# Kernel optimization log

Hardware: AMD Instinct MI355X
Metric: run time of the kernel (lower is better)

Reference implementation:

```python
import jax, jax.numpy as jnp
import numpy as np

DIM = 1280
HEADS = 16
HEAD_DIM = DIM // HEADS  # 80
SEQ = 2048


def setup_inputs() -> dict:
    key = jax.random.key(0)
    ks = jax.random.split(key, 6)
    hidden_states = jax.random.normal(ks[0], (SEQ, DIM), jnp.float32)
    rotary_pos_emb = jax.random.normal(ks[1], (SEQ, HEAD_DIM // 2), jnp.float32)
    # 4 variable-length windows packed into one flat sequence
    cu_seqlens = jnp.array([0, 512, 1024, 1536, 2048], jnp.int32)
    w_scale = DIM ** -0.5
    qkv_w = jax.random.normal(ks[2], (3 * DIM, DIM), jnp.float32) * w_scale
    qkv_b = jax.random.normal(ks[3], (3 * DIM,), jnp.float32) * 0.01
    proj_w = jax.random.normal(ks[4], (DIM, DIM), jnp.float32) * w_scale
    proj_b = jax.random.normal(ks[5], (DIM,), jnp.float32) * 0.01
    return {
        "hidden_states": hidden_states,
        "rotary_pos_emb": rotary_pos_emb,
        "cu_seqlens": cu_seqlens,
        "qkv_w": qkv_w,
        "qkv_b": qkv_b,
        "proj_w": proj_w,
        "proj_b": proj_b,
    }


def _apply_rope_vision(x, freqs):
    # x: [S, H, D], freqs: [S, D//2]; matches Qwen2-VL apply_rotary_pos_emb_vision
    cos = jnp.concatenate([jnp.cos(freqs), jnp.cos(freqs)], axis=-1)[:, None, :]  # [S,1,D]
    sin = jnp.concatenate([jnp.sin(freqs), jnp.sin(freqs)], axis=-1)[:, None, :]
    x1, x2 = jnp.split(x, 2, axis=-1)
    rot = jnp.concatenate([-x2, x1], axis=-1)  # rotate_half
    return x * cos + rot * sin


def reference(hidden_states, rotary_pos_emb, cu_seqlens, qkv_w, qkv_b, proj_w, proj_b):
    S = hidden_states.shape[0]
    qkv = (hidden_states @ qkv_w.T + qkv_b).reshape(S, 3, HEADS, HEAD_DIM)
    q, k, v = qkv[:, 0], qkv[:, 1], qkv[:, 2]  # each [S, H, D]
    q = _apply_rope_vision(q, rotary_pos_emb)
    k = _apply_rope_vision(k, rotary_pos_emb)
    # varlen attention: tokens attend only within their cu_seqlens window
    seg = jnp.searchsorted(cu_seqlens[1:], jnp.arange(S), side="right")
    mask = seg[:, None] == seg[None, :]  # [S, S]
    scale = HEAD_DIM ** -0.5
    scores = jnp.einsum("shd,thd->hst", q, k) * scale  # [H, S, S]
    scores = jnp.where(mask[None, :, :], scores, jnp.finfo(scores.dtype).min)
    probs = jax.nn.softmax(scores, axis=-1)
    attn = jnp.einsum("hst,thd->shd", probs, v).reshape(S, DIM)
    return attn @ proj_w.T + proj_b
```

## Files before the change

kernel.cpp:

```cpp
#include <hip/hip_runtime.h>


typedef __attribute__((ext_vector_type(8))) short bf16x8;
typedef __attribute__((ext_vector_type(4))) float floatx4;
typedef __attribute__((ext_vector_type(4))) short short4v;
typedef __attribute__((ext_vector_type(8))) short short8v;

static __device__ __forceinline__ short f2bf(float f) {
  union { float f; unsigned u; } v; v.f = f;
  unsigned r = v.u + 0x7FFFu + ((v.u >> 16) & 1u);
  return (short)(r >> 16);
}
static __device__ __forceinline__ float bf2f(short h) {
  union { unsigned u; float f; } v;
  v.u = ((unsigned)(unsigned short)h) << 16;
  return v.f;
}

static __device__ __forceinline__ void gload16(const short* g, short* l) {
  __builtin_amdgcn_global_load_lds(
      (const __attribute__((address_space(1))) unsigned*)g,
      (__attribute__((address_space(3))) unsigned*)l, 16, 0, 0);
}

#define CVT_N1 327680
#define CVT_N2 614400
#define CVT_N3 204800
__global__ __launch_bounds__(256) void cvt3_kernel(const float* __restrict__ s1, short* __restrict__ d1,
                                                   const float* __restrict__ s2, short* __restrict__ d2,
                                                   const float* __restrict__ s3, short* __restrict__ d3) {
  int i = blockIdx.x * 256 + threadIdx.x;
  const float* s; short* d; int j;
  if (i < CVT_N1)                { s = s1; d = d1; j = i; }
  else if (i < CVT_N1 + CVT_N2)  { s = s2; d = d2; j = i - CVT_N1; }
  else                           { s = s3; d = d3; j = i - CVT_N1 - CVT_N2; }
  float4 x = ((const float4*)s)[2 * j];
  float4 y = ((const float4*)s)[2 * j + 1];
  short8v o;
  o[0] = f2bf(x.x); o[1] = f2bf(x.y); o[2] = f2bf(x.z); o[3] = f2bf(x.w);
  o[4] = f2bf(y.x); o[5] = f2bf(y.y); o[6] = f2bf(y.z); o[7] = f2bf(y.w);
  ((short8v*)d)[j] = o;
}

template <int MODE, int BM, int BN>
__global__ __launch_bounds__(256) void gemm_lds(const short* __restrict__ A,
                                                const short* __restrict__ B,
                                                const float* __restrict__ bias,
                                                void* __restrict__ Cout,
                                                short* __restrict__ vt,
                                                int M, int N, int K) {
  constexpr int AR = BM / 64;
  constexpr int BR = BN / 64;
  constexpr int MI = BM / 32;
  constexpr int NJ = BN / 32;
  __shared__ short As[BM * 32];
  __shared__ short Bs[BN * 32];

  const int tid = threadIdx.x;
  const int lane = tid & 63;
  const int wave = tid >> 6;
  const int l15 = lane & 15, quad = lane >> 4;

  const short* gA[AR]; short* lA[AR];
#pragma unroll
  for (int r = 0; r < AR; ++r) {
    int ch = r * 256 + tid;
    gA[r] = A + (size_t)(blockIdx.y * BM + (ch >> 2)) * K + (ch & 3) * 8;
    lA[r] = As + ch * 8;
  }
  const short* gB[BR]; short* lB[BR];
#pragma unroll
  for (int r = 0; r < BR; ++r) {
    int ch = r * 256 + tid;
    gB[r] = B + (size_t)(blockIdx.x * BN + (ch >> 2)) * K + (ch & 3) * 8;
    lB[r] = Bs + ch * 8;
  }

  const int wm = (wave >> 1) * (BM / 2);
  const int wn = (wave & 1) * (BN / 2);

  floatx4 acc[MI][NJ];
#pragma unroll
  for (int i = 0; i < MI; ++i)
#pragma unroll
    for (int j = 0; j < NJ; ++j) acc[i][j] = (floatx4){0.f, 0.f, 0.f, 0.f};

  for (int k0 = 0; k0 < K; k0 += 32) {
#pragma unroll
    for (int r = 0; r < AR; ++r) { gload16(gA[r], lA[r]); gA[r] += 32; }
#pragma unroll
    for (int r = 0; r < BR; ++r) { gload16(gB[r], lB[r]); gB[r] += 32; }
    __syncthreads();

    bf16x8 af[MI], bfr[NJ];
#pragma unroll
    for (int i = 0; i < MI; ++i)
      af[i] = *(const bf16x8*)(As + (wm + i * 16 + l15) * 32 + quad * 8);
#pragma unroll
    for (int j = 0; j < NJ; ++j)
      bfr[j] = *(const bf16x8*)(Bs + (wn + j * 16 + l15) * 32 + quad * 8);
#pragma unroll
    for (int i = 0; i < MI; ++i)
#pragma unroll
      for (int j = 0; j < NJ; ++j)
        acc[i][j] = __builtin_amdgcn_mfma_f32_16x16x32_bf16(af[i], bfr[j], acc[i][j], 0, 0, 0);
    __syncthreads();
  }

  const int bm = blockIdx.y * BM + wm;
  const int bn = blockIdx.x * BN + wn;
#pragma unroll
  for (int j = 0; j < NJ; ++j) {
    const int col = bn + j * 16 + l15;
    const float bs = bias[col];
    if (MODE == 1) {
      float* C = (float*)Cout;
#pragma unroll
      for (int i = 0; i < MI; ++i) {
        const int row0 = bm + i * 16 + quad * 4;
#pragma unroll
        for (int e = 0; e < 4; ++e)
          C[(size_t)(row0 + e) * N + col] = acc[i][j][e] + bs;
      }
    } else {
      if (bn + j * 16 < 2560) {
        short* C = (short*)Cout;
#pragma unroll
        for (int i = 0; i < MI; ++i) {
          const int row0 = bm + i * 16 + quad * 4;
#pragma unroll
          for (int e = 0; e < 4; ++e)
            C[(size_t)(row0 + e) * 2560 + col] = f2bf(acc[i][j][e] + bs);
        }
      } else {
#pragma unroll
        for (int i = 0; i < MI; ++i) {
          const int row0 = bm + i * 16 + quad * 4;
          short4v v;
#pragma unroll
          for (int e = 0; e < 4; ++e) v[e] = f2bf(acc[i][j][e] + bs);
          *(short4v*)(vt + (size_t)(col - 2560) * 2048 + row0) = v;
        }
      }
    }
  }
}

__global__ __launch_bounds__(256) void rope_repack(const short* __restrict__ qkv,
                                                   const float* __restrict__ rot,
                                                   short* __restrict__ qp,
                                                   short* __restrict__ kp) {
  int idx = blockIdx.x * 256 + threadIdx.x;
  int d = idx % 96;
  int t = idx / 96;
  int s = t & 2047;
  int h = t >> 11;
  size_t dst = ((size_t)h * 2048 + s) * 96 + d;
  if (d < 80) {
    int base = s * 2560 + h * 80;
    int df = (d < 40) ? d : d - 40;
    int dp = (d < 40) ? d + 40 : d - 40;
    float fr = rot[s * 40 + df];
    float c = __cosf(fr), sn = __sinf(fr);
    float sgn = (d < 40) ? -1.f : 1.f;
    float xq = bf2f(qkv[base + d]);
    float pq = bf2f(qkv[base + dp]);
    float xk = bf2f(qkv[base + 1280 + d]);
    float pk = bf2f(qkv[base + 1280 + dp]);
    qp[dst] = f2bf((xq * c + sgn * pq * sn) * 0.11180339887498949f);
    kp[dst] = f2bf(xk * c + sgn * pk * sn);
  } else {
    qp[dst] = 0;
    kp[dst] = 0;
  }
}

__global__ __launch_bounds__(256) void attn_kernel(const short* __restrict__ qp,
                                                   const short* __restrict__ kp,
                                                   const short* __restrict__ vt,
                                                   short* __restrict__ attnout) {
  __shared__ short smem[29184];
  short* const Ks[2] = {smem, smem + 12288};
  short* const Vs[2] = {smem, smem + 10240};

  const int tid = threadIdx.x;
  const int lane = tid & 63;
  const int wave = tid >> 6;
  const int l15 = lane & 15, quad = lane >> 4;
  short* const Pw = smem + 20480 + wave * (16 * 136);

  const int g = blockIdx.x;
  const int hs = g & 63;
  const int grp = g >> 6;
  const int head = hs >> 2;
  const int seg = hs & 3;
  const int q0 = seg * 512 + (grp * 4 + wave) * 16;

  const short* qb = qp + ((size_t)head * 2048 + q0 + l15) * 96 + quad * 8;
  bf16x8 aq0 = *(const bf16x8*)qb;
  bf16x8 aq1 = *(const bf16x8*)(qb + 32);
  bf16x8 aq2 = *(const bf16x8*)(qb + 64);

  const short* kbase = kp + ((size_t)head * 2048 + seg * 512) * 96;
  const short* vbase = vt + (size_t)head * 80 * 2048 + seg * 512;

  floatx4 s[32];
  {
#pragma unroll
    for (int r = 0; r < 6; ++r) {
      int idx = r * 256 + tid;
      gload16(kbase + idx * 8, Ks[0] + idx * 8);
    }
#pragma unroll
    for (int c = 0; c < 4; ++c) {
      __syncthreads();
      if (c < 3) {
        const short* src = kbase + (size_t)(c + 1) * 128 * 96;
#pragma unroll
        for (int r = 0; r < 6; ++r) {
          int idx = r * 256 + tid;
          gload16(src + idx * 8, Ks[(c + 1) & 1] + idx * 8);
        }
      }
      const short* kl = Ks[c & 1];
#pragma unroll
      for (int j = 0; j < 8; ++j) {
        const short* kb = kl + (j * 16 + l15) * 96 + quad * 8;
        floatx4 acc = (floatx4){0.f, 0.f, 0.f, 0.f};
        acc = __builtin_amdgcn_mfma_f32_16x16x32_bf16(aq0, *(const bf16x8*)kb, acc, 0, 0, 0);
        acc = __builtin_amdgcn_mfma_f32_16x16x32_bf16(aq1, *(const bf16x8*)(kb + 32), acc, 0, 0, 0);
        acc = __builtin_amdgcn_mfma_f32_16x16x32_bf16(aq2, *(const bf16x8*)(kb + 64), acc, 0, 0, 0);
        s[c * 8 + j] = acc;
      }
    }
  }

  float m[4] = {-1e30f, -1e30f, -1e30f, -1e30f};
#pragma unroll
  for (int j = 0; j < 32; ++j)
#pragma unroll
    for (int e = 0; e < 4; ++e) m[e] = fmaxf(m[e], s[j][e]);
#pragma unroll
  for (int e = 0; e < 4; ++e)
#pragma unroll
    for (int o = 1; o < 16; o <<= 1) m[e] = fmaxf(m[e], __shfl_xor(m[e], o));
  float l[4] = {0.f, 0.f, 0.f, 0.f};
#pragma unroll
  for (int j = 0; j < 32; ++j)
#pragma unroll
    for (int e = 0; e < 4; ++e) {
      float p = __expf(s[j][e] - m[e]);
      s[j][e] = p;
      l[e] += p;
    }
#pragma unroll
  for (int e = 0; e < 4; ++e)
#pragma unroll
    for (int o = 1; o < 16; o <<= 1) l[e] += __shfl_xor(l[e], o);
  float inv[4];
#pragma unroll
  for (int e = 0; e < 4; ++e) inv[e] = 1.f / l[e];

  floatx4 o5[5];
#pragma unroll
  for (int t = 0; t < 5; ++t) o5[t] = (floatx4){0.f, 0.f, 0.f, 0.f};

  __syncthreads();
#pragma unroll
  for (int r = 0; r < 5; ++r) {
    int idx = r * 256 + tid;
    gload16(vbase + (size_t)(idx >> 4) * 2048 + (idx & 15) * 8, Vs[0] + idx * 8);
  }
#pragma unroll
  for (int c = 0; c < 4; ++c) {
    __syncthreads();
    if (c < 3) {
      const short* src = vbase + (c + 1) * 128;
#pragma unroll
      for (int r = 0; r < 5; ++r) {
        int idx = r * 256 + tid;
        gload16(src + (size_t)(idx >> 4) * 2048 + (idx & 15) * 8, Vs[(c + 1) & 1] + idx * 8);
      }
    }
#pragma unroll
    for (int j = 0; j < 8; ++j)
#pragma unroll
      for (int e = 0; e < 4; ++e)
        Pw[(quad * 4 + e) * 136 + j * 16 + l15] = f2bf(s[c * 8 + j][e]);
    const short* vl = Vs[c & 1];
#pragma unroll
    for (int kk = 0; kk < 4; ++kk) {
      bf16x8 ap = *(const bf16x8*)&Pw[l15 * 136 + kk * 32 + quad * 8];
#pragma unroll
      for (int t = 0; t < 5; ++t) {
        bf16x8 bv = *(const bf16x8*)&vl[(t * 16 + l15) * 128 + kk * 32 + quad * 8];
        o5[t] = __builtin_amdgcn_mfma_f32_16x16x32_bf16(ap, bv, o5[t], 0, 0, 0);
      }
    }
  }

#pragma unroll
  for (int t = 0; t < 5; ++t)
#pragma unroll
    for (int e = 0; e < 4; ++e)
      attnout[(size_t)(q0 + quad * 4 + e) * 1280 + head * 80 + t * 16 + l15] =
          f2bf(o5[t][e] * inv[e]);
}

extern "C" void kernel_launch(void* const* d_in, const int* in_sizes, int n_in,
                              void* d_out, int out_size, void* d_ws, size_t ws_size,
                              hipStream_t stream) {
  const float* hidden = (const float*)d_in[0];
  const float* rotary = (const float*)d_in[1];
  const float* qkv_w = (const float*)d_in[3];
  const float* qkv_b = (const float*)d_in[4];
  const float* proj_w = (const float*)d_in[5];
  const float* proj_b = (const float*)d_in[6];
  float* out = (float*)d_out;

  char* w = (char*)d_ws;
  short* hA   = (short*)(w + 0);
  short* w1   = (short*)(w + 5242880);
  short* w2   = (short*)(w + 15073280);
  short* qkvb = (short*)(w + 18350080);
  short* qp   = (short*)(w + 28835840);
  short* kp   = (short*)(w + 35127296);
  short* vt   = (short*)(w + 41418752);
  short* attn = (short*)(w + 46661632);

  cvt3_kernel<<<4480, 256, 0, stream>>>(hidden, hA, qkv_w, w1, proj_w, w2);

  gemm_lds<2, 128, 128><<<dim3(3840 / 128, 2048 / 128), 256, 0, stream>>>(
      hA, w1, qkv_b, (void*)qkvb, vt, 2048, 3840, 1280);

  rope_repack<<<16 * 2048 * 96 / 256, 256, 0, stream>>>(qkvb, rotary, qp, kp);

  attn_kernel<<<512, 256, 0, stream>>>(qp, kp, vt, attn);

  gemm_lds<1, 128, 64><<<dim3(1280 / 64, 2048 / 128), 256, 0, stream>>>(
      attn, w2, proj_b, (void*)out, nullptr, 2048, 1280, 1280);
}
```

Baseline: 186.8 us.

## Double-buffer GEMM LDS tiles with K=64 steps, XOR swizzle, smaller tiles

Rewrites the bf16 MFMA GEMM to double-buffer its shared-memory tiles, so the next K slice is fetched with global_load_lds while the current one is consumed. Each K step grows from 32 to 64, and the LDS layout uses an XOR swizzle on 16-byte chunks to avoid bank conflicts. Both GEMM launches switch to BM=64 tiles, giving more blocks for occupancy. The cost is twice the LDS per block and only one barrier per iteration, which relies on the loads completing before the next barrier.

Result: faster. 178.9 us (-4.2%).

```diff
diff --git a/kernel.cpp b/kernel.cpp
--- a/kernel.cpp
+++ b/kernel.cpp
@@ -43,37 +43,36 @@
 }
 
 template <int MODE, int BM, int BN>
-__global__ __launch_bounds__(256) void gemm_lds(const short* __restrict__ A,
-                                                const short* __restrict__ B,
-                                                const float* __restrict__ bias,
-                                                void* __restrict__ Cout,
-                                                short* __restrict__ vt,
-                                                int M, int N, int K) {
-  constexpr int AR = BM / 64;
-  constexpr int BR = BN / 64;
+__global__ __launch_bounds__(256) void gemm_db(const short* __restrict__ A,
+                                               const short* __restrict__ B,
+                                               const float* __restrict__ bias,
+                                               void* __restrict__ Cout,
+                                               short* __restrict__ vt,
+                                               int M, int N, int K) {
+  constexpr int AR = BM / 32;
+  constexpr int BR = BN / 32;
   constexpr int MI = BM / 32;
   constexpr int NJ = BN / 32;
-  __shared__ short As[BM * 32];
-  __shared__ short Bs[BN * 32];
+  __shared__ short As[2][BM * 64];
+  __shared__ short Bs[2][BN * 64];
 
   const int tid = threadIdx.x;
   const int lane = tid & 63;
   const int wave = tid >> 6;
   const int l15 = lane & 15, quad = lane >> 4;
-
-  const short* gA[AR]; short* lA[AR];
+  const int x7 = l15 & 7;
+
+  size_t aoff[AR];
 #pragma unroll
   for (int r = 0; r < AR; ++r) {
-    int ch = r * 256 + tid;
-    gA[r] = A + (size_t)(blockIdx.y * BM + (ch >> 2)) * K + (ch & 3) * 8;
-    lA[r] = As + ch * 8;
-  }
-  const short* gB[BR]; short* lB[BR];
+    int s = r * 256 + tid, row = s >> 3, c = (s & 7) ^ (row & 7);
+    aoff[r] = (size_t)(blockIdx.y * BM + row) * K + c * 8;
+  }
+  size_t boff[BR];
 #pragma unroll
   for (int r = 0; r < BR; ++r) {
-    int ch = r * 256 + tid;
-    gB[r] = B + (size_t)(blockIdx.x * BN + (ch >> 2)) * K + (ch & 3) * 8;
-    lB[r] = Bs + ch * 8;
+    int s = r * 256 + tid, row = s >> 3, c = (s & 7) ^ (row & 7);
+    boff[r] = (size_t)(blockIdx.x * BN + row) * K + c * 8;
   }
 
   const int wm = (wave >> 1) * (BM / 2);
@@ -85,26 +84,42 @@
 #pragma unroll
     for (int j = 0; j < NJ; ++j) acc[i][j] = (floatx4){0.f, 0.f, 0.f, 0.f};
 
-  for (int k0 = 0; k0 < K; k0 += 32) {
-#pragma unroll
-    for (int r = 0; r < AR; ++r) { gload16(gA[r], lA[r]); gA[r] += 32; }
-#pragma unroll
-    for (int r = 0; r < BR; ++r) { gload16(gB[r], lB[r]); gB[r] += 32; }
+#pragma unroll
+  for (int r = 0; r < AR; ++r) gload16(A + aoff[r], &As[0][(r * 256 + tid) * 8]);
+#pragma unroll
+  for (int r = 0; r < BR; ++r) gload16(B + boff[r], &Bs[0][(r * 256 + tid) * 8]);
+
+  int cur = 0;
+  for (int k0 = 0; k0 < K; k0 += 64) {
     __syncthreads();
-
-    bf16x8 af[MI], bfr[NJ];
-#pragma unroll
-    for (int i = 0; i < MI; ++i)
-      af[i] = *(const bf16x8*)(As + (wm + i * 16 + l15) * 32 + quad * 8);
-#pragma unroll
-    for (int j = 0; j < NJ; ++j)
-      bfr[j] = *(const bf16x8*)(Bs + (wn + j * 16 + l15) * 32 + quad * 8);
-#pragma unroll
-    for (int i = 0; i < MI; ++i)
-#pragma unroll
-      for (int j = 0; j < NJ; ++j)
-        acc[i][j] = __builtin_amdgcn_mfma_f32_16x16x32_bf16(af[i], bfr[j], acc[i][j], 0, 0, 0);
-    __syncthreads();
+    if (k0 + 64 < K) {
+#pragma unroll
+      for (int r = 0; r < AR; ++r)
+        gload16(A + aoff[r] + k0 + 64, &As[cur ^ 1][(r * 256 + tid) * 8]);
+#pragma unroll
+      for (int r = 0; r < BR; ++r)
+        gload16(B + boff[r] + k0 + 64, &Bs[cur ^ 1][(r * 256 + tid) * 8]);
+    }
+#pragma unroll
+    for (int h = 0; h < 2; ++h) {
+      bf16x8 af[MI], bfr[NJ];
+#pragma unroll
+      for (int i = 0; i < MI; ++i) {
+        int row = wm + i * 16 + l15;
+        af[i] = *(const bf16x8*)&As[cur][row * 64 + (((h << 2) + quad) ^ x7) * 8];
+      }
+#pragma unroll
+      for (int j = 0; j < NJ; ++j) {
+        int row = wn + j * 16 + l15;
+        bfr[j] = *(const bf16x8*)&Bs[cur][row * 64 + (((h << 2) + quad) ^ x7) * 8];
+      }
+#pragma unroll
+      for (int i = 0; i < MI; ++i)
+#pragma unroll
+        for (int j = 0; j < NJ; ++j)
+          acc[i][j] = __builtin_amdgcn_mfma_f32_16x16x32_bf16(af[i], bfr[j], acc[i][j], 0, 0, 0);
+    }
+    cur ^= 1;
   }
 
   const int bm = blockIdx.y * BM + wm;
@@ -330,13 +345,13 @@
 
   cvt3_kernel<<<4480, 256, 0, stream>>>(hidden, hA, qkv_w, w1, proj_w, w2);
 
-  gemm_lds<2, 128, 128><<<dim3(3840 / 128, 2048 / 128), 256, 0, stream>>>(
+  gemm_db<2, 64, 128><<<dim3(3840 / 128, 2048 / 64), 256, 0, stream>>>(
       hA, w1, qkv_b, (void*)qkvb, vt, 2048, 3840, 1280);
 
   rope_repack<<<16 * 2048 * 96 / 256, 256, 0, stream>>>(qkvb, rotary, qp, kp);
 
   attn_kernel<<<512, 256, 0, stream>>>(qp, kp, vt, attn);
 
-  gemm_lds<1, 128, 64><<<dim3(1280 / 64, 2048 / 128), 256, 0, stream>>>(
+  gemm_db<1, 64, 64><<<dim3(1280 / 64, 2048 / 64), 256, 0, stream>>>(
       attn, w2, proj_b, (void*)out, nullptr, 2048, 1280, 1280);
 }
```
